# Kernel tuning notes

Hardware: AMD Instinct MI355X
Metric: run time of the kernel (lower is better)

Reference implementation:

```python
import jax, jax.numpy as jnp
import numpy as np
from jax import lax

# Mamba-130m style config (overrides per init_kwargs)
N_LAYERS = 8
D_MODEL = 768
D_IN = 1536            # intermediate_size
N_STATE = 16           # state_size
DT_RANK = 48           # time_step_rank
K_CONV = 4             # conv_kernel
VOCAB = 1024
EPS = 1e-5


def setup_inputs() -> dict:
    key = jax.random.key(0)
    ks = jax.random.split(key, 16)
    L, B = 1024, 1
    src = jax.random.randint(ks[0], (L, B), 0, VOCAB, dtype=jnp.int64)
    s = 0.02
    embed = jax.random.normal(ks[1], (VOCAB, D_MODEL), jnp.float32) * s
    norm_w = jnp.ones((N_LAYERS, D_MODEL), jnp.float32)
    in_proj_w = jax.random.normal(ks[2], (N_LAYERS, 2 * D_IN, D_MODEL), jnp.float32) * s
    conv_w = jax.random.normal(ks[3], (N_LAYERS, D_IN, K_CONV), jnp.float32) * 0.1
    conv_b = jnp.zeros((N_LAYERS, D_IN), jnp.float32)
    x_proj_w = jax.random.normal(ks[4], (N_LAYERS, DT_RANK + 2 * N_STATE, D_IN), jnp.float32) * s
    dt_proj_w = jax.random.normal(ks[5], (N_LAYERS, D_IN, DT_RANK), jnp.float32) * s
    # HF init: dt bias ~ inv_softplus of dt in [1e-3, 1e-1]; a small negative bias keeps dt sane
    dt_proj_b = jax.random.uniform(ks[6], (N_LAYERS, D_IN), jnp.float32, -4.0, -2.0)
    # HF init: A = 1..N repeated over channels; A_log = log(A)
    A_log = jnp.log(jnp.broadcast_to(jnp.arange(1, N_STATE + 1, dtype=jnp.float32), (N_LAYERS, D_IN, N_STATE)))
    D_param = jnp.ones((N_LAYERS, D_IN), jnp.float32)
    out_proj_w = jax.random.normal(ks[7], (N_LAYERS, D_MODEL, D_IN), jnp.float32) * s
    final_norm_w = jnp.ones((D_MODEL,), jnp.float32)
    lm_head_w = embed  # HF Mamba ties lm_head to embeddings
    return dict(src=src, embed=embed, norm_w=norm_w, in_proj_w=in_proj_w,
                conv_w=conv_w, conv_b=conv_b, x_proj_w=x_proj_w,
                dt_proj_w=dt_proj_w, dt_proj_b=dt_proj_b, A_log=A_log,
                D_param=D_param, out_proj_w=out_proj_w,
                final_norm_w=final_norm_w, lm_head_w=lm_head_w)


def _rmsnorm(x, w):
    var = jnp.mean(jnp.square(x), axis=-1, keepdims=True)
    return x * jax.lax.rsqrt(var + EPS) * w


def _mamba_forward(src, embed, norm_w, in_proj_w, conv_w, conv_b, x_proj_w,
                   dt_proj_w, dt_proj_b, A_log, D_param, out_proj_w,
                   final_norm_w, lm_head_w):
    # src: [L, B] -> input_ids [B, L]
    ids = src.T  # [B, L]
    x = embed[ids]  # [B, L, D]
    Bsz, L, _ = x.shape

    def layer_step(h_in, lp):
        (nw, iw, cw, cb, xw, dtw, dtb, alog, dpar, ow) = lp
        res = h_in
        h = _rmsnorm(h_in, nw)
        proj = jnp.einsum('bld,ed->ble', h, iw)      # [B,L,2*D_IN]
        u, gate = jnp.split(proj, 2, axis=-1)
        # depthwise causal conv over time
        u_c = jnp.transpose(u, (0, 2, 1))            # [B,D_IN,L]
        u_c = lax.conv_general_dilated(
            u_c, cw[:, None, :], (1,), [(K_CONV - 1, 0)],
            feature_group_count=D_IN,
            dimension_numbers=('NCH', 'OIH', 'NCH')) + cb[None, :, None]
        u = jax.nn.silu(jnp.transpose(u_c, (0, 2, 1)))   # [B,L,D_IN]
        xdb = jnp.einsum('bld,ed->ble', u, xw)           # [B,L,DT_RANK+2N]
        dt_in = xdb[..., :DT_RANK]
        B_ssm = xdb[..., DT_RANK:DT_RANK + N_STATE]      # [B,L,N]
        C_ssm = xdb[..., DT_RANK + N_STATE:]             # [B,L,N]
        dt = jax.nn.softplus(jnp.einsum('blr,dr->bld', dt_in, dtw) + dtb)  # [B,L,D_IN]
        A = -jnp.exp(alog)                               # [D_IN,N]

        def scan_step(hs, inp):
            dt_t, B_t, C_t, u_t = inp                    # [B,D_IN],[B,N],[B,N],[B,D_IN]
            dA = jnp.exp(dt_t[..., None] * A)            # [B,D_IN,N]
            hs = dA * hs + (dt_t * u_t)[..., None] * B_t[:, None, :]
            y = jnp.einsum('bdn,bn->bd', hs, C_t)
            return hs, y

        h0 = jnp.zeros((Bsz, D_IN, N_STATE), x.dtype)
        xs = (jnp.swapaxes(dt, 0, 1), jnp.swapaxes(B_ssm, 0, 1),
              jnp.swapaxes(C_ssm, 0, 1), jnp.swapaxes(u, 0, 1))
        _, ys = lax.scan(scan_step, h0, xs)              # ys: [L,B,D_IN]
        y = jnp.swapaxes(ys, 0, 1) + u * dpar            # skip term u * D
        y = y * jax.nn.silu(gate)
        out = jnp.einsum('ble,de->bld', y, ow)
        return res + out, None

    layer_params = (norm_w, in_proj_w, conv_w, conv_b, x_proj_w,
                    dt_proj_w, dt_proj_b, A_log, D_param, out_proj_w)
    x, _ = lax.scan(layer_step, x, layer_params)
    x = _rmsnorm(x, final_norm_w)
    logits = jnp.einsum('bld,vd->blv', x, lm_head_w)     # [B,L,V]
    return jnp.transpose(logits, (1, 0, 2))              # [L,B,V] (forward transposes back)


def reference(src, embed, norm_w, in_proj_w, conv_w, conv_b, x_proj_w,
              dt_proj_w, dt_proj_b, A_log, D_param, out_proj_w,
              final_norm_w, lm_head_w):
    return _mamba_forward(src, embed, norm_w, in_proj_w, conv_w, conv_b,
                          x_proj_w, dt_proj_w, dt_proj_b, A_log, D_param,
                          out_proj_w, final_norm_w, lm_head_w)
```

## Files before the change

### kernel.cpp

```cpp
#include <hip/hip_runtime.h>
#include <math.h>

#define DM 768
#define DIN 1536
#define NST 16
#define DTR 48
#define LSEQ 1024
#define NLAYERS 8
#define VOCAB_ 1024
#define CHUNK 16
#define NCHUNK 64

typedef __attribute__((ext_vector_type(4))) float  f32x4;
typedef __attribute__((ext_vector_type(8))) unsigned short u16x8;
typedef __attribute__((ext_vector_type(8))) __bf16 bf16x8;

__device__ __forceinline__ float sigmoidf_(float x){ return 1.f/(1.f+__expf(-x)); }

__device__ __forceinline__ unsigned short f2bf(float x){
  union { float f; unsigned u; } a; a.f = x;
  unsigned r = a.u + 0x7FFFu + ((a.u >> 16) & 1u);
  return (unsigned short)(r >> 16);
}
__device__ __forceinline__ float bfhi2f(unsigned short h){
  union { unsigned u; float f; } a; a.u = ((unsigned)h) << 16; return a.f;
}

__device__ __forceinline__ f32x4 mfma_bf16(u16x8 a, u16x8 b, f32x4 c){
  return __builtin_amdgcn_mfma_f32_16x16x32_bf16(
      __builtin_bit_cast(bf16x8, a), __builtin_bit_cast(bf16x8, b), c, 0, 0, 0);
}

__device__ __forceinline__ void gload16(const unsigned short* g, unsigned short* l){
  __builtin_amdgcn_global_load_lds(
      (const __attribute__((address_space(1))) void*)g,
      (__attribute__((address_space(3))) void*)l, 16, 0, 0);
}

__global__ __launch_bounds__(256) void k_embed(const int* __restrict__ src, const float* __restrict__ emb, float* __restrict__ x){
  int l = blockIdx.x; int id = src[l];
  const float* e = emb + (size_t)id*DM;
  float* o = x + (size_t)l*DM;
  for (int i = threadIdx.x; i < DM; i += 256) o[i] = e[i];
}

__global__ __launch_bounds__(256) void k_rmsnorm3(const float* __restrict__ x, const float* __restrict__ w, unsigned short* __restrict__ o3){
  int l = blockIdx.x; int t = threadIdx.x;
  const float* xr = x + (size_t)l*DM;
  float v0 = xr[t], v1 = xr[t+256], v2 = xr[t+512];
  float p = v0*v0 + v1*v1 + v2*v2;
  #pragma unroll
  for (int m = 32; m >= 1; m >>= 1) p += __shfl_xor(p, m);
  __shared__ float red[4];
  if ((t & 63) == 0) red[t >> 6] = p;
  __syncthreads();
  float tot = red[0]+red[1]+red[2]+red[3];
  float s = rsqrtf(tot * (1.f/DM) + 1e-5f);
  size_t b = (size_t)l*(3*DM);
  float vv[3] = { v0*s*w[t], v1*s*w[t+256], v2*s*w[t+512] };
  int cc[3] = { t, t+256, t+512 };
  #pragma unroll
  for (int i=0;i<3;i++){
    unsigned short hi = f2bf(vv[i]);
    o3[b + cc[i]]        = hi;
    o3[b + DM + cc[i]]   = f2bf(vv[i] - bfhi2f(hi));
    o3[b + 2*DM + cc[i]] = hi;
  }
}

__global__ __launch_bounds__(256) void k_cvt3wv(const float* __restrict__ W, unsigned short* __restrict__ O,
                                                int K, int K3p, int Nr){
  int k8 = (blockIdx.x*256 + threadIdx.x) * 8;
  int r = blockIdx.y;
  if (k8 >= K) return;
  const bool valid = (r < Nr);
  f32x4 a = valid ? *(const f32x4*)&W[(size_t)r*K + k8]     : (f32x4){0,0,0,0};
  f32x4 b = valid ? *(const f32x4*)&W[(size_t)r*K + k8 + 4] : (f32x4){0,0,0,0};
  u16x8 h, lo;
  #pragma unroll
  for (int j=0;j<4;j++){
    h[j] = f2bf(a[j]);   lo[j]   = f2bf(a[j] - bfhi2f(h[j]));
    h[4+j] = f2bf(b[j]); lo[4+j] = f2bf(b[j] - bfhi2f(h[4+j]));
  }
  size_t base = (size_t)r*K3p;
  *(u16x8*)&O[base + k8]       = h;
  *(u16x8*)&O[base + K + k8]   = h;
  *(u16x8*)&O[base + 2*K + k8] = lo;
  int pad = K3p - 3*K;
  if (k8 < pad) *(u16x8*)&O[base + 3*K + k8] = (u16x8){0,0,0,0,0,0,0,0};
}

template<int EPI>
__global__ __launch_bounds__(256) void k_gemm3(
    const unsigned short* __restrict__ A3,
    const unsigned short* __restrict__ B3,
    float* __restrict__ C, const float* __restrict__ aux,
    int K3, int strideK, int ldc, int N)
{
  __shared__ unsigned short As[2][64*64];
  __shared__ unsigned short Bs[2][64*64];
  const int tid = threadIdx.x, lane = tid & 63, wave = tid >> 6;
  const int id = blockIdx.x;
  const int cpx = gridDim.x >> 3;
  const int wg = (id & 7)*cpx + (id >> 3);
  const int m0 = (wg & 15) * 64, n0 = (wg >> 4) * 64;
  const int wm = wave >> 1, wn = wave & 1;
  const int frow = lane & 15, kg = lane >> 4;
  const size_t kco = (size_t)blockIdx.z * K3;
  C += (size_t)blockIdx.z * 1024 * ldc;

  const int srow = lane >> 3;
  const int ssw  = (lane & 7) ^ srow;
  const unsigned short* gA = A3 + (size_t)(m0 + wave*16 + srow)*strideK + kco + ssw*8;
  const unsigned short* gB = B3 + (size_t)(n0 + wave*16 + srow)*strideK + kco + ssw*8;
  const int lbase = (wave*16)*64;

  f32x4 acc[2][2];
  #pragma unroll
  for (int i=0;i<2;i++){ acc[i][0]=(f32x4){0,0,0,0}; acc[i][1]=(f32x4){0,0,0,0}; }

  const int nt = K3 >> 6;
  #pragma unroll
  for (int i=0;i<2;i++){
    gload16(gA + (size_t)i*8*strideK, &As[0][lbase + i*8*64]);
    gload16(gB + (size_t)i*8*strideK, &Bs[0][lbase + i*8*64]);
  }
  __syncthreads();

  int cur = 0;
  for (int t = 0; t < nt; ++t){
    if (t+1 < nt){
      const unsigned short* a = gA + (size_t)(t+1)*64;
      const unsigned short* b = gB + (size_t)(t+1)*64;
      #pragma unroll
      for (int i=0;i<2;i++){
        gload16(a + (size_t)i*8*strideK, &As[cur^1][lbase + i*8*64]);
        gload16(b + (size_t)i*8*strideK, &Bs[cur^1][lbase + i*8*64]);
      }
    }
    const unsigned short* Ab = &As[cur][0];
    const unsigned short* Bb = &Bs[cur][0];
    #pragma unroll
    for (int c=0;c<2;c++){
      u16x8 fa[2], fb[2];
      #pragma unroll
      for (int i=0;i<2;i++){
        const int ra = wm*32 + i*16 + frow;
        const int xa = (c*64 + kg*16) ^ ((ra & 7) << 4);
        fa[i] = *(const u16x8*)&Ab[ra*64 + (xa >> 1)];
        const int rb = wn*32 + i*16 + frow;
        const int xb = (c*64 + kg*16) ^ ((rb & 7) << 4);
        fb[i] = *(const u16x8*)&Bb[rb*64 + (xb >> 1)];
      }
      #pragma unroll
      for (int mi=0;mi<2;mi++)
        #pragma unroll
        for (int ni=0;ni<2;ni++)
          acc[mi][ni] = mfma_bf16(fa[mi], fb[ni], acc[mi][ni]);
    }
    __syncthreads();
    cur ^= 1;
  }

  #pragma unroll
  for (int mi=0;mi<2;mi++){
    #pragma unroll
    for (int ni=0;ni<2;ni++){
      const int col = n0 + wn*32 + ni*16 + frow;
      #pragma unroll
      for (int rr=0;rr<4;rr++){
        const int row = m0 + wm*32 + mi*16 + kg*4 + rr;
        float v = acc[mi][ni][rr];
        if (EPI == 0){
          C[(size_t)row*ldc + col] = v;
        } else if (EPI == 1){
          v += aux[col];
          C[(size_t)row*ldc + col] = (v > 20.f) ? v : log1pf(__expf(v));
        } else if (EPI == 2){
          C[(size_t)row*ldc + col] = v + aux[(size_t)row*ldc + col];
        }
      }
    }
  }
}

__global__ __launch_bounds__(256) void k_redo(float* __restrict__ x, const float* __restrict__ p){
  int i = blockIdx.x*256 + threadIdx.x;
  f32x4 a = *(const f32x4*)&p[(size_t)i*4];
  f32x4 b = *(const f32x4*)&p[(size_t)i*4 + 786432];
  f32x4 xv = *(const f32x4*)&x[(size_t)i*4];
  xv += a + b;
  *(f32x4*)&x[(size_t)i*4] = xv;
}

__global__ __launch_bounds__(256) void k_redx(const float* __restrict__ Pp,
    unsigned short* __restrict__ dtin3, float* __restrict__ xbc){
  int idx = blockIdx.x*256 + threadIdx.x;
  if (idx >= 1024*80) return;
  int row = idx / 80, col = idx - row*80;
  float s = 0.f;
  #pragma unroll
  for (int k=0;k<8;k++) s += Pp[(size_t)k*1024*128 + row*128 + col];
  if (col < 48){
    unsigned short hi = f2bf(s);
    size_t b = (size_t)row*192;
    dtin3[b + col]       = hi;
    dtin3[b + 48 + col]  = f2bf(s - bfhi2f(hi));
    dtin3[b + 96 + col]  = hi;
    dtin3[b + 144 + col] = 0;
  } else {
    xbc[(size_t)row*32 + (col - 48)] = s;
  }
}

__global__ __launch_bounds__(256) void k_conv(const float* __restrict__ proj, const float* __restrict__ cw, const float* __restrict__ cb,
                                              float* __restrict__ u, unsigned short* __restrict__ u3){
  int c = blockIdx.x*256 + threadIdx.x;
  int l = blockIdx.y;
  float w0=cw[c*4+0], w1=cw[c*4+1], w2=cw[c*4+2], w3=cw[c*4+3];
  float s = cb[c];
  s += proj[(size_t)l*3072 + c] * w3;
  if (l >= 1) s += proj[(size_t)(l-1)*3072 + c] * w2;
  if (l >= 2) s += proj[(size_t)(l-2)*3072 + c] * w1;
  if (l >= 3) s += proj[(size_t)(l-3)*3072 + c] * w0;
  float v = s * sigmoidf_(s);
  u[(size_t)l*DIN + c] = v;
  size_t b = (size_t)l*(3*DIN);
  unsigned short hi = f2bf(v);
  u3[b + c]         = hi;
  u3[b + DIN + c]   = f2bf(v - bfhi2f(hi));
  u3[b + 2*DIN + c] = hi;
}

__global__ __launch_bounds__(256) void k_scan1(
  const float* __restrict__ dt, const float* __restrict__ u,
  const float* __restrict__ xbc, float* __restrict__ P, float* __restrict__ H)
{
  __shared__ float Bsh[CHUNK][NST];
  int t = threadIdx.x;
  int d = blockIdx.x*256 + t;
  int chunk = blockIdx.y;
  int l0 = chunk * CHUNK;
  { int l = t >> 4, n = t & 15; Bsh[l][n] = xbc[(size_t)(l0+l)*32 + n]; }
  __syncthreads();
  float h[NST]; float sdt = 0.f;
  #pragma unroll
  for (int n=0;n<NST;n++) h[n]=0.f;
  for (int l=0;l<CHUNK;l++){
    float dtv = dt[(size_t)(l0+l)*DIN + d];
    float uv  = u[(size_t)(l0+l)*DIN + d];
    float du = dtv*uv;
    float e1 = __expf(-dtv);
    float en = e1;
    #pragma unroll
    for (int n=0;n<NST;n++){ h[n] = en*h[n] + du*Bsh[l][n]; en *= e1; }
    sdt += dtv;
  }
  float p1 = __expf(-sdt), pn = p1;
  #pragma unroll
  for (int n=0;n<NST;n++){
    P[(size_t)(chunk*NST+n)*DIN + d] = pn;
    H[(size_t)(chunk*NST+n)*DIN + d] = h[n];
    pn *= p1;
  }
}

__global__ __launch_bounds__(256) void k_scan2(float* __restrict__ P, const float* __restrict__ H){
  int i = blockIdx.x*256 + threadIdx.x;
  float s = 0.f;
  #pragma unroll 8
  for (int c=0;c<NCHUNK;c++){
    size_t off = (size_t)c*(NST*DIN) + i;
    float p = P[off], hh = H[off];
    P[off] = s;
    s = p*s + hh;
  }
}

__global__ __launch_bounds__(256) void k_scan3(
  const float* __restrict__ dt, const float* __restrict__ u,
  const float* __restrict__ xbc, const float* __restrict__ Sin,
  const float* __restrict__ proj, const float* __restrict__ Dp,
  unsigned short* __restrict__ y3)
{
  __shared__ float Bsh[CHUNK][NST];
  __shared__ float Csh[CHUNK][NST];
  int t = threadIdx.x;
  int d = blockIdx.x*256 + t;
  int chunk = blockIdx.y;
  int l0 = chunk * CHUNK;
  { int l = t >> 4, n = t & 15;
    Bsh[l][n] = xbc[(size_t)(l0+l)*32 + n];
    Csh[l][n] = xbc[(size_t)(l0+l)*32 + 16 + n]; }
  __syncthreads();
  float h[NST];
  #pragma unroll
  for (int n=0;n<NST;n++) h[n] = Sin[(size_t)(chunk*NST+n)*DIN + d];
  float Dv = Dp[d];
  for (int l=0;l<CHUNK;l++){
    float dtv = dt[(size_t)(l0+l)*DIN + d];
    float uv  = u[(size_t)(l0+l)*DIN + d];
    float du = dtv*uv;
    float e1 = __expf(-dtv);
    float en = e1;
    float yv = 0.f;
    #pragma unroll
    for (int n=0;n<NST;n++){
      h[n] = en*h[n] + du*Bsh[l][n];
      yv += h[n]*Csh[l][n];
      en *= e1;
    }
    yv += uv*Dv;
    float g = proj[(size_t)(l0+l)*3072 + DIN + d];
    float v = yv * g * sigmoidf_(g);
    size_t b = (size_t)(l0+l)*(3*DIN);
    unsigned short hi = f2bf(v);
    y3[b + d]         = hi;
    y3[b + DIN + d]   = f2bf(v - bfhi2f(hi));
    y3[b + 2*DIN + d] = hi;
  }
}

extern "C" void kernel_launch(void* const* d_in, const int* in_sizes, int n_in,
                              void* d_out, int out_size, void* d_ws, size_t ws_size,
                              hipStream_t stream)
{
  const int*   src        = (const int*)d_in[0];
  const float* embed      = (const float*)d_in[1];
  const float* norm_w     = (const float*)d_in[2];
  const float* in_proj_w  = (const float*)d_in[3];
  const float* conv_w     = (const float*)d_in[4];
  const float* conv_b     = (const float*)d_in[5];
  const float* x_proj_w   = (const float*)d_in[6];
  const float* dt_proj_w  = (const float*)d_in[7];
  const float* dt_proj_b  = (const float*)d_in[8];
  const float* D_param    = (const float*)d_in[10];
  const float* out_proj_w = (const float*)d_in[11];
  const float* final_norm_w = (const float*)d_in[12];
  const float* lm_head_w  = (const float*)d_in[13];
  float* out = (float*)d_out;

  float* ws = (float*)d_ws;
  size_t off = 0;
  auto alloc = [&](size_t n){ float* p = ws + off; off += (n + 63) & ~size_t(63); return p; };
  auto alloc3 = [&](size_t nush){ return (unsigned short*)alloc((nush + 1) / 2); };

  float* x     = alloc((size_t)LSEQ*DM);
  float* proj  = alloc((size_t)LSEQ*3072);
  float* u     = alloc((size_t)LSEQ*DIN);
  float* xdbBC = alloc((size_t)LSEQ*32);
  float* dtb   = alloc((size_t)LSEQ*DIN);
  float* P     = alloc((size_t)NCHUNK*NST*DIN);
  float* Hc    = alloc((size_t)NCHUNK*NST*DIN);
  float* Pp    = alloc((size_t)8*1024*128);
  float* Pout  = alloc((size_t)2*1024*768);
  unsigned short* act3  = alloc3((size_t)LSEQ*4608);
  unsigned short* dtin3 = alloc3((size_t)LSEQ*192);
  unsigned short* inW3  = alloc3((size_t)3072*2304);
  unsigned short* xpW3  = alloc3((size_t)128*4608);
  unsigned short* dtW3  = alloc3((size_t)1536*192);
  unsigned short* outW3 = alloc3((size_t)768*4608);
  unsigned short* lmW3  = alloc3((size_t)1024*2304);

  k_embed<<<LSEQ, 256, 0, stream>>>(src, embed, x);

  for (int layer = 0; layer < NLAYERS; ++layer) {
    k_cvt3wv<<<dim3(1, 3072), 256, 0, stream>>>(in_proj_w + (size_t)layer*3072*DM, inW3, DM, 2304, 3072);
    k_rmsnorm3<<<LSEQ, 256, 0, stream>>>(x, norm_w + (size_t)layer*DM, act3);
    k_gemm3<0><<<16*48, 256, 0, stream>>>(act3, inW3, proj, nullptr, 2304, 2304, 3072, 3072);
    k_conv<<<dim3(DIN/256, LSEQ), 256, 0, stream>>>(proj, conv_w + (size_t)layer*DIN*4, conv_b + (size_t)layer*DIN, u, act3);
    k_cvt3wv<<<dim3(1, 128), 256, 0, stream>>>(x_proj_w + (size_t)layer*80*DIN, xpW3, DIN, 4608, 80);
    k_gemm3<0><<<dim3(32, 1, 8), 256, 0, stream>>>(act3, xpW3, Pp, nullptr, 576, 4608, 128, 128);
    k_redx<<<320, 256, 0, stream>>>(Pp, dtin3, xdbBC);
    k_cvt3wv<<<dim3(1, 1536), 256, 0, stream>>>(dt_proj_w + (size_t)layer*DIN*DTR, dtW3, DTR, 192, 1536);
    k_gemm3<1><<<16*24, 256, 0, stream>>>(dtin3, dtW3, dtb, dt_proj_b + (size_t)layer*DIN, 192, 192, 1536, 1536);
    k_scan1<<<dim3(DIN/256, NCHUNK), 256, 0, stream>>>(dtb, u, xdbBC, P, Hc);
    k_scan2<<<(NST*DIN)/256, 256, 0, stream>>>(P, Hc);
    k_scan3<<<dim3(DIN/256, NCHUNK), 256, 0, stream>>>(dtb, u, xdbBC, P, proj, D_param + (size_t)layer*DIN, act3);
    k_cvt3wv<<<dim3(1, 768), 256, 0, stream>>>(out_proj_w + (size_t)layer*DM*DIN, outW3, DIN, 4608, 768);
    k_gemm3<0><<<dim3(16*12, 1, 2), 256, 0, stream>>>(act3, outW3, Pout, nullptr, 2304, 4608, 768, 768);
    k_redo<<<768, 256, 0, stream>>>(x, Pout);
  }

  k_rmsnorm3<<<LSEQ, 256, 0, stream>>>(x, final_norm_w, act3);
  k_cvt3wv<<<dim3(1, 1024), 256, 0, stream>>>(lm_head_w, lmW3, DM, 2304, 1024);
  k_gemm3<0><<<16*16, 256, 0, stream>>>(act3, lmW3, out, nullptr, 2304, 2304, VOCAB_, VOCAB_);
}
```

Baseline: 1.038 ms.

## Widen GEMM tiles to 64x128 and fuse per-layer weight conversions

The GEMM kernel gains an NB template parameter so each block computes a 64x(64*NB) output tile. A-tile loads are reused across two B sub-tiles, which halves A traffic and the block count for the in_proj, dt_proj, out_proj and lm_head GEMMs. The four per-layer weight split-bf16 conversion launches are merged into one kernel to cut launch overhead. Larger tiles raise register and LDS use and leave fewer blocks for 256 CUs, so occupancy on the smaller GEMMs may suffer.

```diff
diff --git a/kernel.cpp b/kernel.cpp
--- a/kernel.cpp
+++ b/kernel.cpp
@@ -68,6 +68,37 @@
   }
 }
 
+__global__ __launch_bounds__(256) void k_cvtL(
+    const float* __restrict__ inW, const float* __restrict__ xpW,
+    const float* __restrict__ dtW, const float* __restrict__ outW,
+    unsigned short* __restrict__ Oin, unsigned short* __restrict__ Oxp,
+    unsigned short* __restrict__ Odt, unsigned short* __restrict__ Oout)
+{
+  int z = blockIdx.y;
+  const float* W; unsigned short* O; int K, K3p, Nr, r;
+  if (z < 3072)      { r = z;        W = inW;  O = Oin;  K = 768;  K3p = 2304; Nr = 3072; }
+  else if (z < 3200) { r = z - 3072; W = xpW;  O = Oxp;  K = 1536; K3p = 4608; Nr = 80;   }
+  else if (z < 4736) { r = z - 3200; W = dtW;  O = Odt;  K = 48;   K3p = 192;  Nr = 1536; }
+  else               { r = z - 4736; W = outW; O = Oout; K = 1536; K3p = 4608; Nr = 768;  }
+  int k8 = threadIdx.x * 8;
+  if (k8 >= K) return;
+  const bool valid = (r < Nr);
+  f32x4 a = valid ? *(const f32x4*)&W[(size_t)r*K + k8]     : (f32x4){0,0,0,0};
+  f32x4 b = valid ? *(const f32x4*)&W[(size_t)r*K + k8 + 4] : (f32x4){0,0,0,0};
+  u16x8 h, lo;
+  #pragma unroll
+  for (int j=0;j<4;j++){
+    h[j] = f2bf(a[j]);   lo[j]   = f2bf(a[j] - bfhi2f(h[j]));
+    h[4+j] = f2bf(b[j]); lo[4+j] = f2bf(b[j] - bfhi2f(h[4+j]));
+  }
+  size_t base = (size_t)r*K3p;
+  *(u16x8*)&O[base + k8]       = h;
+  *(u16x8*)&O[base + K + k8]   = h;
+  *(u16x8*)&O[base + 2*K + k8] = lo;
+  int pad = K3p - 3*K;
+  if (k8 < pad) *(u16x8*)&O[base + 3*K + k8] = (u16x8){0,0,0,0,0,0,0,0};
+}
+
 __global__ __launch_bounds__(256) void k_cvt3wv(const float* __restrict__ W, unsigned short* __restrict__ O,
                                                 int K, int K3p, int Nr){
   int k8 = (blockIdx.x*256 + threadIdx.x) * 8;
@@ -90,7 +121,7 @@
   if (k8 < pad) *(u16x8*)&O[base + 3*K + k8] = (u16x8){0,0,0,0,0,0,0,0};
 }
 
-template<int EPI>
+template<int EPI, int NB>
 __global__ __launch_bounds__(256) void k_gemm3(
     const unsigned short* __restrict__ A3,
     const unsigned short* __restrict__ B3,
@@ -98,12 +129,12 @@
     int K3, int strideK, int ldc, int N)
 {
   __shared__ unsigned short As[2][64*64];
-  __shared__ unsigned short Bs[2][64*64];
+  __shared__ unsigned short Bs[2][NB][64*64];
   const int tid = threadIdx.x, lane = tid & 63, wave = tid >> 6;
   const int id = blockIdx.x;
   const int cpx = gridDim.x >> 3;
   const int wg = (id & 7)*cpx + (id >> 3);
-  const int m0 = (wg & 15) * 64, n0 = (wg >> 4) * 64;
+  const int m0 = (wg & 15) * 64, n0 = (wg >> 4) * (64*NB);
   const int wm = wave >> 1, wn = wave & 1;
   const int frow = lane & 15, kg = lane >> 4;
   const size_t kco = (size_t)blockIdx.z * K3;
@@ -112,50 +143,60 @@
   const int srow = lane >> 3;
   const int ssw  = (lane & 7) ^ srow;
   const unsigned short* gA = A3 + (size_t)(m0 + wave*16 + srow)*strideK + kco + ssw*8;
-  const unsigned short* gB = B3 + (size_t)(n0 + wave*16 + srow)*strideK + kco + ssw*8;
+  const unsigned short* gB[NB];
+  #pragma unroll
+  for (int nb=0; nb<NB; ++nb)
+    gB[nb] = B3 + (size_t)(n0 + nb*64 + wave*16 + srow)*strideK + kco + ssw*8;
   const int lbase = (wave*16)*64;
 
-  f32x4 acc[2][2];
-  #pragma unroll
-  for (int i=0;i<2;i++){ acc[i][0]=(f32x4){0,0,0,0}; acc[i][1]=(f32x4){0,0,0,0}; }
+  f32x4 acc[2][2*NB];
+  #pragma unroll
+  for (int i=0;i<2;i++)
+    #pragma unroll
+    for (int j=0;j<2*NB;j++) acc[i][j] = (f32x4){0,0,0,0};
 
   const int nt = K3 >> 6;
   #pragma unroll
   for (int i=0;i<2;i++){
     gload16(gA + (size_t)i*8*strideK, &As[0][lbase + i*8*64]);
-    gload16(gB + (size_t)i*8*strideK, &Bs[0][lbase + i*8*64]);
+    #pragma unroll
+    for (int nb=0; nb<NB; ++nb)
+      gload16(gB[nb] + (size_t)i*8*strideK, &Bs[0][nb][lbase + i*8*64]);
   }
   __syncthreads();
 
   int cur = 0;
   for (int t = 0; t < nt; ++t){
     if (t+1 < nt){
-      const unsigned short* a = gA + (size_t)(t+1)*64;
-      const unsigned short* b = gB + (size_t)(t+1)*64;
       #pragma unroll
       for (int i=0;i<2;i++){
-        gload16(a + (size_t)i*8*strideK, &As[cur^1][lbase + i*8*64]);
-        gload16(b + (size_t)i*8*strideK, &Bs[cur^1][lbase + i*8*64]);
+        gload16(gA + (size_t)(t+1)*64 + (size_t)i*8*strideK, &As[cur^1][lbase + i*8*64]);
+        #pragma unroll
+        for (int nb=0; nb<NB; ++nb)
+          gload16(gB[nb] + (size_t)(t+1)*64 + (size_t)i*8*strideK, &Bs[cur^1][nb][lbase + i*8*64]);
       }
     }
-    const unsigned short* Ab = &As[cur][0];
-    const unsigned short* Bb = &Bs[cur][0];
     #pragma unroll
     for (int c=0;c<2;c++){
-      u16x8 fa[2], fb[2];
+      u16x8 fa[2], fb[2*NB];
       #pragma unroll
       for (int i=0;i<2;i++){
         const int ra = wm*32 + i*16 + frow;
         const int xa = (c*64 + kg*16) ^ ((ra & 7) << 4);
-        fa[i] = *(const u16x8*)&Ab[ra*64 + (xa >> 1)];
-        const int rb = wn*32 + i*16 + frow;
+        fa[i] = *(const u16x8*)&As[cur][ra*64 + (xa >> 1)];
+      }
+      #pragma unroll
+      for (int j=0;j<2*NB;j++){
+        const int nloc = wn*32*NB + j*16;
+        const int nb = nloc >> 6;
+        const int rb = (nloc & 63) + frow;
         const int xb = (c*64 + kg*16) ^ ((rb & 7) << 4);
-        fb[i] = *(const u16x8*)&Bb[rb*64 + (xb >> 1)];
+        fb[j] = *(const u16x8*)&Bs[cur][nb][rb*64 + (xb >> 1)];
       }
       #pragma unroll
       for (int mi=0;mi<2;mi++)
         #pragma unroll
-        for (int ni=0;ni<2;ni++)
+        for (int ni=0;ni<2*NB;ni++)
           acc[mi][ni] = mfma_bf16(fa[mi], fb[ni], acc[mi][ni]);
     }
     __syncthreads();
@@ -165,8 +206,8 @@
   #pragma unroll
   for (int mi=0;mi<2;mi++){
     #pragma unroll
-    for (int ni=0;ni<2;ni++){
-      const int col = n0 + wn*32 + ni*16 + frow;
+    for (int ni=0;ni<2*NB;ni++){
+      const int col = n0 + wn*32*NB + ni*16 + frow;
       #pragma unroll
       for (int rr=0;rr<4;rr++){
         const int row = m0 + wm*32 + mi*16 + kg*4 + rr;
@@ -365,24 +406,24 @@
   k_embed<<<LSEQ, 256, 0, stream>>>(src, embed, x);
 
   for (int layer = 0; layer < NLAYERS; ++layer) {
-    k_cvt3wv<<<dim3(1, 3072), 256, 0, stream>>>(in_proj_w + (size_t)layer*3072*DM, inW3, DM, 2304, 3072);
+    k_cvtL<<<dim3(1, 5504), 256, 0, stream>>>(
+        in_proj_w + (size_t)layer*3072*DM, x_proj_w + (size_t)layer*80*DIN,
+        dt_proj_w + (size_t)layer*DIN*DTR, out_proj_w + (size_t)layer*DM*DIN,
+        inW3, xpW3, dtW3, outW3);
     k_rmsnorm3<<<LSEQ, 256, 0, stream>>>(x, norm_w + (size_t)layer*DM, act3);
-    k_gemm3<0><<<16*48, 256, 0, stream>>>(act3, inW3, proj, nullptr, 2304, 2304, 3072, 3072);
+    k_gemm3<0,2><<<16*24, 256, 0, stream>>>(act3, inW3, proj, nullptr, 2304, 2304, 3072, 3072);
     k_conv<<<dim3(DIN/256, LSEQ), 256, 0, stream>>>(proj, conv_w + (size_t)layer*DIN*4, conv_b + (size_t)layer*DIN, u, act3);
-    k_cvt3wv<<<dim3(1, 128), 256, 0, stream>>>(x_proj_w + (size_t)layer*80*DIN, xpW3, DIN, 4608, 80);
-    k_gemm3<0><<<dim3(32, 1, 8), 256, 0, stream>>>(act3, xpW3, Pp, nullptr, 576, 4608, 128, 128);
+    k_gemm3<0,1><<<dim3(32, 1, 8), 256, 0, stream>>>(act3, xpW3, Pp, nullptr, 576, 4608, 128, 128);
     k_redx<<<320, 256, 0, stream>>>(Pp, dtin3, xdbBC);
-    k_cvt3wv<<<dim3(1, 1536), 256, 0, stream>>>(dt_proj_w + (size_t)layer*DIN*DTR, dtW3, DTR, 192, 1536);
-    k_gemm3<1><<<16*24, 256, 0, stream>>>(dtin3, dtW3, dtb, dt_proj_b + (size_t)layer*DIN, 192, 192, 1536, 1536);
+    k_gemm3<1,2><<<16*12, 256, 0, stream>>>(dtin3, dtW3, dtb, dt_proj_b + (size_t)layer*DIN, 192, 192, 1536, 1536);
     k_scan1<<<dim3(DIN/256, NCHUNK), 256, 0, stream>>>(dtb, u, xdbBC, P, Hc);
     k_scan2<<<(NST*DIN)/256, 256, 0, stream>>>(P, Hc);
     k_scan3<<<dim3(DIN/256, NCHUNK), 256, 0, stream>>>(dtb, u, xdbBC, P, proj, D_param + (size_t)layer*DIN, act3);
-    k_cvt3wv<<<dim3(1, 768), 256, 0, stream>>>(out_proj_w + (size_t)layer*DM*DIN, outW3, DIN, 4608, 768);
-    k_gemm3<0><<<dim3(16*12, 1, 2), 256, 0, stream>>>(act3, outW3, Pout, nullptr, 2304, 4608, 768, 768);
+    k_gemm3<0,2><<<dim3(16*6, 1, 2), 256, 0, stream>>>(act3, outW3, Pout, nullptr, 2304, 4608, 768, 768);
     k_redo<<<768, 256, 0, stream>>>(x, Pout);
   }
 
   k_rmsnorm3<<<LSEQ, 256, 0, stream>>>(x, final_norm_w, act3);
   k_cvt3wv<<<dim3(1, 1024), 256, 0, stream>>>(lm_head_w, lmW3, DM, 2304, 1024);
-  k_gemm3<0><<<16*16, 256, 0, stream>>>(act3, lmW3, out, nullptr, 2304, 2304, VOCAB_, VOCAB_);
-}
+  k_gemm3<0,2><<<16*8, 256, 0, stream>>>(act3, lmW3, out, nullptr, 2304, 2304, VOCAB_, VOCAB_);
+}
```

New measurement: 1.166 ms. +12.4%, slower.
